# Kernel tuning notes

Hardware: AMD Instinct MI355X
Metric: run time of the kernel (lower is better)

Reference implementation:

```python
import jax, jax.numpy as jnp
import numpy as np

D_MODEL = 1024
NUM_HEADS = 16
D_HEAD = D_MODEL // NUM_HEADS
THETA = 10000.0
NEG_INF = -1e9


def apply_rope(x, theta=THETA):
    # x: (..., S, Dh) with interleaved pairs (2i, 2i+1)
    S, Dh = x.shape[-2], x.shape[-1]
    inv_freq = 1.0 / (theta ** (jnp.arange(0, Dh, 2, dtype=jnp.float32) / Dh))  # (Dh/2,)
    ang = jnp.arange(S, dtype=jnp.float32)[:, None] * inv_freq[None, :]          # (S, Dh/2)
    cos, sin = jnp.cos(ang), jnp.sin(ang)
    x1 = x[..., 0::2]
    x2 = x[..., 1::2]
    r1 = x1 * cos - x2 * sin
    r2 = x1 * sin + x2 * cos
    # interleave back
    return jnp.stack([r1, r2], axis=-1).reshape(x.shape)


def setup_inputs() -> dict:
    key = jax.random.key(0)
    ks = jax.random.split(key, 5)
    B, S = 2, 2048
    scale = 1.0 / np.sqrt(D_MODEL)
    return {
        "x": jax.random.normal(ks[0], (B, S, D_MODEL), dtype=jnp.float32),
        "Wq": jax.random.normal(ks[1], (D_MODEL, D_MODEL), dtype=jnp.float32) * scale,
        "Wk": jax.random.normal(ks[2], (D_MODEL, D_MODEL), dtype=jnp.float32) * scale,
        "Wv": jax.random.normal(ks[3], (D_MODEL, D_MODEL), dtype=jnp.float32) * scale,
        "Wo": jax.random.normal(ks[4], (D_MODEL, D_MODEL), dtype=jnp.float32) * scale,
    }


def reference(x, Wq, Wk, Wv, Wo):
    B, S, _ = x.shape
    def split_heads(t):
        return t.reshape(B, S, NUM_HEADS, D_HEAD).transpose(0, 2, 1, 3)  # (B,H,S,Dh)
    # nn.Linear(bias=False): y = x @ W.T
    Q = split_heads(x @ Wq.T)
    K = split_heads(x @ Wk.T)
    V = split_heads(x @ Wv.T)
    Q = apply_rope(Q)
    K = apply_rope(K)
    scale = 1.0 / jnp.sqrt(jnp.asarray(D_HEAD, dtype=x.dtype))
    scores = jnp.einsum("bhqd,bhkd->bhqk", Q, K) * scale  # (B,H,S,S)
    causal = jnp.tril(jnp.ones((S, S), dtype=bool))
    scores = jnp.where(causal, scores, NEG_INF)
    attn = jax.nn.softmax(scores, axis=-1)
    out = jnp.einsum("bhqk,bhkd->bhqd", attn, V)
    out = out.transpose(0, 2, 1, 3).reshape(B, S, D_MODEL)
    return out @ Wo.T
```

## Files before the change

### kernel.cpp

```cpp
#include <hip/hip_runtime.h>
#include <hip/hip_bf16.h>
#include <stdint.h>

typedef __attribute__((ext_vector_type(8))) short bf8;
typedef __attribute__((ext_vector_type(4))) float f4;

#define MFMA16(a, b, c) __builtin_amdgcn_mfma_f32_16x16x32_bf16((a), (b), (c), 0, 0, 0)

static __device__ __forceinline__ short f2b(float f) {
  uint32_t x = __float_as_uint(f);
  x += 0x7fffu + ((x >> 16) & 1u);
  return (short)(x >> 16);
}

static __device__ __forceinline__ uint32_t pk2(float a, float b) {
  return ((__float_as_uint(a) + 0x8000u) >> 16) |
         ((__float_as_uint(b) + 0x8000u) & 0xffff0000u);
}

static __device__ __forceinline__ void gload16(const short* g, void* l) {
  __builtin_amdgcn_global_load_lds(
      (const __attribute__((address_space(1))) void*)g,
      (__attribute__((address_space(3))) void*)l, 16, 0, 0);
}

__global__ void convert_kernel(const float* __restrict__ x,
                               const float* __restrict__ wq, const float* __restrict__ wk,
                               const float* __restrict__ wv, const float* __restrict__ wo,
                               short* __restrict__ xb, short* __restrict__ Wb,
                               float2* __restrict__ tab) {
  const int bid = blockIdx.x;
  if (bid >= 4096) {
    const int t = (bid - 4096) * 256 + threadIdx.x;
    const int s = t >> 5, i = t & 31;
    const float inv = powf(10000.0f, -(float)i * (1.0f / 32.0f));
    const float ang = (float)s * inv;
    float sv, cv;
    sincosf(ang, &sv, &cv);
    tab[t] = make_float2(cv, sv);
    return;
  }
  const size_t i = ((size_t)bid * 256 + threadIdx.x) * 8;
  const float* __restrict__ src;
  short* __restrict__ dst;
  if (i < 4194304u) {
    src = x + i;
    dst = xb + i;
  } else {
    const size_t j = i - 4194304u;
    const int z = (int)(j >> 20);
    const size_t o = j & 1048575u;
    src = (z == 0 ? wq : z == 1 ? wk : z == 2 ? wv : wo) + o;
    dst = Wb + j;
  }
  const float4 a = *(const float4*)src;
  const float4 b = *(const float4*)(src + 4);
  bf8 v;
  v[0] = f2b(a.x); v[1] = f2b(a.y); v[2] = f2b(a.z); v[3] = f2b(a.w);
  v[4] = f2b(b.x); v[5] = f2b(b.y); v[6] = f2b(b.z); v[7] = f2b(b.w);
  *(bf8*)dst = v;
}

template <int MODE>
__launch_bounds__(256, 2)
__global__ void gemm_kernel(const short* __restrict__ Ab, const short* __restrict__ Wb,
                            short* __restrict__ Qo, short* __restrict__ Ko,
                            short* __restrict__ VTo, float* __restrict__ Fo,
                            const float2* __restrict__ rope) {
  constexpr int K = 1024;
  const int bm = blockIdx.x, bn = blockIdx.y;
  const int z = (MODE == 0) ? blockIdx.z : 3;
  const short* __restrict__ Bb = Wb + ((size_t)z << 20);

  __shared__ short As[128 * 64];
  __shared__ short Bs[128 * 64];

  const int tid = threadIdx.x;
  const int lane = tid & 63;
  const int wave = tid >> 6;
  const int wr = wave >> 1, wc = wave & 1;
  const int lg = lane >> 4, lr = lane & 15;

  f4 acc[4][4];
#pragma unroll
  for (int i = 0; i < 4; i++)
#pragma unroll
    for (int j = 0; j < 4; j++) {
      acc[i][j][0] = 0.f; acc[i][j][1] = 0.f;
      acc[i][j][2] = 0.f; acc[i][j][3] = 0.f;
    }

  const int kc = tid & 7;
  const int srow = tid >> 3;
  const int kcs = (kc ^ (srow & 7)) * 8;
  char* const Asw = (char*)As + wave * 1024;
  char* const Bsw = (char*)Bs + wave * 1024;

  for (int k0 = 0; k0 < K; k0 += 64) {
#pragma unroll
    for (int i = 0; i < 4; i++) {
      const int row = srow + i * 32;
      gload16(Ab + (size_t)(bm * 128 + row) * K + k0 + kcs, Asw + i * 4096);
      gload16(Bb + (size_t)(bn * 128 + row) * K + k0 + kcs, Bsw + i * 4096);
    }
    __syncthreads();
#pragma unroll
    for (int kk = 0; kk < 2; kk++) {
      bf8 af[4], bb[4];
#pragma unroll
      for (int mi = 0; mi < 4; mi++) {
        const int row = wr * 64 + mi * 16 + lr;
        const int lb = (row * 128 + kk * 64 + lg * 16) ^ ((row & 7) << 4);
        af[mi] = *(const bf8*)((const char*)As + lb);
      }
#pragma unroll
      for (int ni = 0; ni < 4; ni++) {
        const int row = wc * 64 + ni * 16 + lr;
        const int lb = (row * 128 + kk * 64 + lg * 16) ^ ((row & 7) << 4);
        bb[ni] = *(const bf8*)((const char*)Bs + lb);
      }
#pragma unroll
      for (int mi = 0; mi < 4; mi++)
#pragma unroll
        for (int ni = 0; ni < 4; ni++)
          acc[mi][ni] = MFMA16(af[mi], bb[ni], acc[mi][ni]);
    }
    __syncthreads();
  }

  if (MODE == 1) {
#pragma unroll
    for (int mi = 0; mi < 4; mi++) {
      const int m0 = bm * 128 + wr * 64 + mi * 16 + lg * 4;
#pragma unroll
      for (int ni = 0; ni < 4; ni++) {
        const int n = bn * 128 + wc * 64 + ni * 16 + lr;
#pragma unroll
        for (int r = 0; r < 4; r++)
          Fo[(size_t)(m0 + r) * 1024 + n] = acc[mi][ni][r];
      }
    }
    return;
  }

  if (z == 2) {
#pragma unroll
    for (int mi = 0; mi < 4; mi++) {
      const int m0 = bm * 128 + wr * 64 + mi * 16 + lg * 4;
      const int b = m0 >> 11, s0 = m0 & 2047;
#pragma unroll
      for (int ni = 0; ni < 4; ni++) {
        const int n = bn * 128 + wc * 64 + ni * 16 + lr;
        ushort4 pk;
        pk.x = (unsigned short)f2b(acc[mi][ni][0]);
        pk.y = (unsigned short)f2b(acc[mi][ni][1]);
        pk.z = (unsigned short)f2b(acc[mi][ni][2]);
        pk.w = (unsigned short)f2b(acc[mi][ni][3]);
        *(ushort4*)(VTo + ((size_t)((b * 16 + (n >> 6)) * 64 + (n & 63))) * 2048 + s0) = pk;
      }
    }
  } else {
    short* __restrict__ Out = (z == 0) ? Qo : Ko;
    const float qscale = (z == 0) ? 0.18033688011112042f : 1.0f;
#pragma unroll
    for (int mi = 0; mi < 4; mi++) {
      const int m0 = bm * 128 + wr * 64 + mi * 16 + lg * 4;
      const int b = m0 >> 11, s0 = m0 & 2047;
#pragma unroll
      for (int ni = 0; ni < 4; ni++) {
        const int n = bn * 128 + wc * 64 + ni * 16 + lr;
        const int h = n >> 6, d = n & 63;
        const float sgn = (d & 1) ? 1.0f : -1.0f;
#pragma unroll
        for (int r = 0; r < 4; r++) {
          const float v = acc[mi][ni][r];
          const float p = __shfl_xor(v, 1);
          const float2 cs = rope[((s0 + r) << 5) + (d >> 1)];
          const float res = (v * cs.x + sgn * p * cs.y) * qscale;
          Out[((size_t)(b * 16 + h) * 2048 + (s0 + r)) * 64 + d] = f2b(res);
        }
      }
    }
  }
}

__launch_bounds__(512, 4)
__global__ void attn_kernel(const short* __restrict__ Qg, const short* __restrict__ Kg,
                            const short* __restrict__ Vg, short* __restrict__ AO) {
  const int S = 2048;
  const int id = blockIdx.x;
  const int xcd = id & 7, slot = id >> 3;
  const int bh = xcd * 4 + (slot & 3);
  const int u = id >> 5;
  const int qb = (u < 8) ? (15 - 2 * u) : (2 * u - 16);
  const int tid = threadIdx.x;
  const int lane = tid & 63, wave = tid >> 6;
  const int lg = lane >> 4, lr = lane & 15;
  const short* __restrict__ Qp = Qg + (size_t)bh * S * 64;
  const short* __restrict__ Kp = Kg + (size_t)bh * S * 64;
  const short* __restrict__ Vp = Vg + (size_t)bh * 64 * S;

  __shared__ short KB[2][64 * 64];
  __shared__ short VB[2][64 * 64];
  __shared__ short PB[8][16 * 64];

  const int srow = tid >> 3;
  const int kcs = ((tid & 7) ^ (srow & 7)) * 8;
  const size_t ksrc = (size_t)srow * 64 + kcs;
  const size_t vsrc = (size_t)srow * 2048 + kcs;

  const int qbase = qb * 128 + wave * 16;
  const int my_nkv = (qbase + 79) >> 6;
  const int blk_nkv = (qb * 128 + 191) >> 6;

  bf8 qf[2];
#pragma unroll
  for (int ks = 0; ks < 2; ks++)
    qf[ks] = *(const bf8*)(Qp + (size_t)(qbase + lr) * 64 + ks * 32 + lg * 8);

  f4 o[4];
#pragma unroll
  for (int dt = 0; dt < 4; dt++) {
    o[dt][0] = 0.f; o[dt][1] = 0.f; o[dt][2] = 0.f; o[dt][3] = 0.f;
  }
  float mrun = -1e30f, lsum = 0.f;

  char* const Pw = (char*)&PB[wave][0];
  const int rowoff = lr * 128;
  const int sw = (lr & 7) << 4;

  gload16(Kp + ksrc, (char*)KB[0] + wave * 1024);
  gload16(Vp + vsrc, (char*)VB[0] + wave * 1024);
  __syncthreads();

  for (int kb = 0; kb < blk_nkv; kb++) {
    const int kvb = kb * 64;
    const int cur = kb & 1;

    if (kb + 1 < blk_nkv) {
      gload16(Kp + (size_t)(kvb + 64) * 64 + ksrc, (char*)KB[cur ^ 1] + wave * 1024);
      gload16(Vp + (size_t)(kvb + 64) + vsrc, (char*)VB[cur ^ 1] + wave * 1024);
    }

    if (kb < my_nkv) {
      const char* Kc = (const char*)KB[cur];
      const char* Vc = (const char*)VB[cur];

      f4 st[4];
      __builtin_amdgcn_s_setprio(1);
#pragma unroll
      for (int nt = 0; nt < 4; nt++) {
        const int row = nt * 16 + lr;
        const int base = row * 128 + lg * 16;
        const int rsw = (row & 7) << 4;
        const bf8 k0 = *(const bf8*)(Kc + ((base) ^ rsw));
        const bf8 k1 = *(const bf8*)(Kc + ((base + 64) ^ rsw));
        f4 c;
        c[0] = 0.f; c[1] = 0.f; c[2] = 0.f; c[3] = 0.f;
        c = MFMA16(k0, qf[0], c);
        c = MFMA16(k1, qf[1], c);
        st[nt] = c;
      }
      __builtin_amdgcn_s_setprio(0);

      if ((kvb + 63) > qbase) {
        const int q = qbase + lr;
#pragma unroll
        for (int nt = 0; nt < 4; nt++)
#pragma unroll
          for (int r = 0; r < 4; r++) {
            const int kv = kvb + nt * 16 + lg * 4 + r;
            if (kv > q) st[nt][r] = -1e9f;
          }
      }

      float m0 = fmaxf(fmaxf(st[0][0], st[0][1]), fmaxf(st[0][2], st[0][3]));
#pragma unroll
      for (int nt = 1; nt < 4; nt++)
        m0 = fmaxf(m0, fmaxf(fmaxf(st[nt][0], st[nt][1]), fmaxf(st[nt][2], st[nt][3])));
      m0 = fmaxf(m0, __shfl_xor(m0, 16));
      m0 = fmaxf(m0, __shfl_xor(m0, 32));

      if (__any(m0 - mrun > 8.0f)) {
        const float mn = fmaxf(mrun, m0);
        const float corr = __builtin_amdgcn_exp2f(mrun - mn);
        mrun = mn;
        lsum *= corr;
#pragma unroll
        for (int r = 0; r < 4; r++) {
          const float co = __shfl(corr, (lg << 2) + r);
#pragma unroll
          for (int dt = 0; dt < 4; dt++) o[dt][r] *= co;
        }
      }

      asm volatile("s_waitcnt lgkmcnt(0)" ::: "memory");

#pragma unroll
      for (int nt = 0; nt < 4; nt++) {
        const float p0 = __builtin_amdgcn_exp2f(st[nt][0] - mrun);
        const float p1 = __builtin_amdgcn_exp2f(st[nt][1] - mrun);
        const float p2 = __builtin_amdgcn_exp2f(st[nt][2] - mrun);
        const float p3 = __builtin_amdgcn_exp2f(st[nt][3] - mrun);
        lsum += (p0 + p1) + (p2 + p3);
        *(uint2*)(Pw + ((rowoff + nt * 32 + lg * 8) ^ sw)) = make_uint2(pk2(p0, p1), pk2(p2, p3));
      }

      asm volatile("s_waitcnt lgkmcnt(0)" ::: "memory");

      bf8 pf[2];
#pragma unroll
      for (int ks = 0; ks < 2; ks++)
        pf[ks] = *(const bf8*)(Pw + ((rowoff + ks * 64 + lg * 16) ^ sw));

      __builtin_amdgcn_s_setprio(1);
#pragma unroll
      for (int dt = 0; dt < 4; dt++) {
        const int row = dt * 16 + lr;
        const int base = row * 128 + lg * 16;
        const int rsw = (row & 7) << 4;
        const bf8 v0 = *(const bf8*)(Vc + ((base) ^ rsw));
        const bf8 v1 = *(const bf8*)(Vc + ((base + 64) ^ rsw));
        o[dt] = MFMA16(pf[0], v0, o[dt]);
        o[dt] = MFMA16(pf[1], v1, o[dt]);
      }
      __builtin_amdgcn_s_setprio(0);
    }

    __syncthreads();
  }

  float s = lsum;
  s += __shfl_xor(s, 16);
  s += __shfl_xor(s, 32);
  const float inv = 1.0f / s;
  float inv_o[4];
#pragma unroll
  for (int r = 0; r < 4; r++) inv_o[r] = __shfl(inv, (lg << 2) + r);

  const int b = bh >> 4, h = bh & 15;
#pragma unroll
  for (int r = 0; r < 4; r++) {
    const int q = qbase + lg * 4 + r;
#pragma unroll
    for (int dt = 0; dt < 4; dt++) {
      const int d = dt * 16 + lr;
      AO[((size_t)b * 2048 + q) * 1024 + h * 64 + d] = f2b(o[dt][r] * inv_o[r]);
    }
  }
}

extern "C" void kernel_launch(void* const* d_in, const int* in_sizes, int n_in,
                              void* d_out, int out_size, void* d_ws, size_t ws_size,
                              hipStream_t stream) {
  const float* x  = (const float*)d_in[0];
  const float* wq = (const float*)d_in[1];
  const float* wk = (const float*)d_in[2];
  const float* wv = (const float*)d_in[3];
  const float* wo = (const float*)d_in[4];
  float* out = (float*)d_out;

  char* ws = (char*)d_ws;
  short*  Qb  = (short*)(ws);
  short*  Kb  = (short*)(ws + (8ull  << 20));
  short*  VTb = (short*)(ws + (16ull << 20));
  short*  AOb = (short*)(ws + (24ull << 20));
  short*  xb  = AOb;
  short*  Wb  = (short*)(ws + (32ull << 20));
  float2* tab = (float2*)(ws + (40ull << 20));

  convert_kernel<<<4352, 256, 0, stream>>>(x, wq, wk, wv, wo, xb, Wb, tab);
  gemm_kernel<0><<<dim3(32, 8, 3), 256, 0, stream>>>(
      xb, Wb, Qb, Kb, VTb, nullptr, tab);
  attn_kernel<<<512, 512, 0, stream>>>(Qb, Kb, VTb, AOb);
  gemm_kernel<1><<<dim3(32, 8, 1), 256, 0, stream>>>(
      AOb, Wb, nullptr, nullptr, nullptr, out, nullptr);
}
```

Baseline: 114.1 us.

## Rewrite attention with 32x32 MFMA, register-resident P via permlane swap

The attention kernel switches from 16x16x32 MFMAs with a shared-memory round trip for the probability tile to 32x32x16 MFMAs. The P tile stays in registers and is rearranged into operand layout with v_permlane32_swap. Blocks shrink to two waves covering 64 query rows each, with a 1024-block grid ordered heaviest-first. The aim is to cut LDS traffic and waits and raise MFMA efficiency. The cost is more accumulator registers and smaller blocks, each doing more K/V staging per wave.

```diff
diff --git a/kernel.cpp b/kernel.cpp
--- a/kernel.cpp
+++ b/kernel.cpp
@@ -4,8 +4,11 @@
 
 typedef __attribute__((ext_vector_type(8))) short bf8;
 typedef __attribute__((ext_vector_type(4))) float f4;
+typedef __attribute__((ext_vector_type(16))) float f16f;
+typedef __attribute__((ext_vector_type(4))) unsigned int u32x4;
 
 #define MFMA16(a, b, c) __builtin_amdgcn_mfma_f32_16x16x32_bf16((a), (b), (c), 0, 0, 0)
+#define MFMA32(a, b, c) __builtin_amdgcn_mfma_f32_32x32x16_bf16((a), (b), (c), 0, 0, 0)
 
 static __device__ __forceinline__ short f2b(float f) {
   uint32_t x = __float_as_uint(f);
@@ -16,6 +19,13 @@
 static __device__ __forceinline__ uint32_t pk2(float a, float b) {
   return ((__float_as_uint(a) + 0x8000u) >> 16) |
          ((__float_as_uint(b) + 0x8000u) & 0xffff0000u);
+}
+
+static __device__ __forceinline__ bf8 mk_bf8(uint32_t w0, uint32_t w1,
+                                             uint32_t w2, uint32_t w3) {
+  union { u32x4 u; bf8 b; } t;
+  t.u = (u32x4){w0, w1, w2, w3};
+  return t.b;
 }
 
 static __device__ __forceinline__ void gload16(const short* g, void* l) {
@@ -184,170 +194,157 @@
   }
 }
 
-__launch_bounds__(512, 4)
+__launch_bounds__(128, 2)
 __global__ void attn_kernel(const short* __restrict__ Qg, const short* __restrict__ Kg,
                             const short* __restrict__ Vg, short* __restrict__ AO) {
   const int S = 2048;
   const int id = blockIdx.x;
-  const int xcd = id & 7, slot = id >> 3;
-  const int bh = xcd * 4 + (slot & 3);
-  const int u = id >> 5;
-  const int qb = (u < 8) ? (15 - 2 * u) : (2 * u - 16);
+  const int xcd = id & 7;
+  const int rest = id >> 3;
+  const int bh = xcd * 4 + (rest & 3);
+  const int qt = 31 - (rest >> 2);
   const int tid = threadIdx.x;
   const int lane = tid & 63, wave = tid >> 6;
-  const int lg = lane >> 4, lr = lane & 15;
+  const int l31 = lane & 31, hi = lane >> 5;
   const short* __restrict__ Qp = Qg + (size_t)bh * S * 64;
   const short* __restrict__ Kp = Kg + (size_t)bh * S * 64;
   const short* __restrict__ Vp = Vg + (size_t)bh * 64 * S;
 
   __shared__ short KB[2][64 * 64];
   __shared__ short VB[2][64 * 64];
-  __shared__ short PB[8][16 * 64];
-
-  const int srow = tid >> 3;
-  const int kcs = ((tid & 7) ^ (srow & 7)) * 8;
-  const size_t ksrc = (size_t)srow * 64 + kcs;
-  const size_t vsrc = (size_t)srow * 2048 + kcs;
-
-  const int qbase = qb * 128 + wave * 16;
-  const int my_nkv = (qbase + 79) >> 6;
-  const int blk_nkv = (qb * 128 + 191) >> 6;
-
-  bf8 qf[2];
-#pragma unroll
-  for (int ks = 0; ks < 2; ks++)
-    qf[ks] = *(const bf8*)(Qp + (size_t)(qbase + lr) * 64 + ks * 32 + lg * 8);
-
-  f4 o[4];
-#pragma unroll
-  for (int dt = 0; dt < 4; dt++) {
-    o[dt][0] = 0.f; o[dt][1] = 0.f; o[dt][2] = 0.f; o[dt][3] = 0.f;
-  }
+
+  const int qbase = qt * 64 + wave * 32;
+  const int nkv = qt + 1;
+
+  const int srow = lane >> 3;
+  const int chsw = ((lane & 7) ^ srow) * 8;
+
+#define STAGE(buf, kvb_)                                                          \
+  do {                                                                            \
+    _Pragma("unroll") for (int c = 0; c < 4; c++) {                               \
+      const int rr = wave * 32 + c * 8 + srow;                                    \
+      gload16(Kp + (size_t)((kvb_) + rr) * 64 + chsw,                             \
+              (char*)KB[buf] + (wave * 32 + c * 8) * 128);                        \
+      gload16(Vp + (size_t)rr * 2048 + (kvb_) + chsw,                             \
+              (char*)VB[buf] + (wave * 32 + c * 8) * 128);                        \
+    }                                                                             \
+  } while (0)
+
+  bf8 qf[4];
+#pragma unroll
+  for (int ks = 0; ks < 4; ks++)
+    qf[ks] = *(const bf8*)(Qp + (size_t)(qbase + l31) * 64 + ks * 16 + hi * 8);
+
+  f16f o0, o1;
+#pragma unroll
+  for (int i = 0; i < 16; i++) { o0[i] = 0.f; o1[i] = 0.f; }
   float mrun = -1e30f, lsum = 0.f;
 
-  char* const Pw = (char*)&PB[wave][0];
-  const int rowoff = lr * 128;
-  const int sw = (lr & 7) << 4;
-
-  gload16(Kp + ksrc, (char*)KB[0] + wave * 1024);
-  gload16(Vp + vsrc, (char*)VB[0] + wave * 1024);
+  const int rsw = (l31 & 7) << 4;
+
+  STAGE(0, 0);
   __syncthreads();
 
-  for (int kb = 0; kb < blk_nkv; kb++) {
+  for (int kb = 0; kb < nkv; kb++) {
     const int kvb = kb * 64;
     const int cur = kb & 1;
 
-    if (kb + 1 < blk_nkv) {
-      gload16(Kp + (size_t)(kvb + 64) * 64 + ksrc, (char*)KB[cur ^ 1] + wave * 1024);
-      gload16(Vp + (size_t)(kvb + 64) + vsrc, (char*)VB[cur ^ 1] + wave * 1024);
-    }
-
-    if (kb < my_nkv) {
-      const char* Kc = (const char*)KB[cur];
-      const char* Vc = (const char*)VB[cur];
-
-      f4 st[4];
-      __builtin_amdgcn_s_setprio(1);
-#pragma unroll
-      for (int nt = 0; nt < 4; nt++) {
-        const int row = nt * 16 + lr;
-        const int base = row * 128 + lg * 16;
-        const int rsw = (row & 7) << 4;
-        const bf8 k0 = *(const bf8*)(Kc + ((base) ^ rsw));
-        const bf8 k1 = *(const bf8*)(Kc + ((base + 64) ^ rsw));
-        f4 c;
-        c[0] = 0.f; c[1] = 0.f; c[2] = 0.f; c[3] = 0.f;
-        c = MFMA16(k0, qf[0], c);
-        c = MFMA16(k1, qf[1], c);
-        st[nt] = c;
-      }
-      __builtin_amdgcn_s_setprio(0);
-
-      if ((kvb + 63) > qbase) {
-        const int q = qbase + lr;
-#pragma unroll
-        for (int nt = 0; nt < 4; nt++)
-#pragma unroll
-          for (int r = 0; r < 4; r++) {
-            const int kv = kvb + nt * 16 + lg * 4 + r;
-            if (kv > q) st[nt][r] = -1e9f;
-          }
-      }
-
-      float m0 = fmaxf(fmaxf(st[0][0], st[0][1]), fmaxf(st[0][2], st[0][3]));
-#pragma unroll
-      for (int nt = 1; nt < 4; nt++)
-        m0 = fmaxf(m0, fmaxf(fmaxf(st[nt][0], st[nt][1]), fmaxf(st[nt][2], st[nt][3])));
-      m0 = fmaxf(m0, __shfl_xor(m0, 16));
-      m0 = fmaxf(m0, __shfl_xor(m0, 32));
-
-      if (__any(m0 - mrun > 8.0f)) {
-        const float mn = fmaxf(mrun, m0);
-        const float corr = __builtin_amdgcn_exp2f(mrun - mn);
-        mrun = mn;
-        lsum *= corr;
-#pragma unroll
-        for (int r = 0; r < 4; r++) {
-          const float co = __shfl(corr, (lg << 2) + r);
-#pragma unroll
-          for (int dt = 0; dt < 4; dt++) o[dt][r] *= co;
-        }
-      }
-
-      asm volatile("s_waitcnt lgkmcnt(0)" ::: "memory");
-
-#pragma unroll
-      for (int nt = 0; nt < 4; nt++) {
-        const float p0 = __builtin_amdgcn_exp2f(st[nt][0] - mrun);
-        const float p1 = __builtin_amdgcn_exp2f(st[nt][1] - mrun);
-        const float p2 = __builtin_amdgcn_exp2f(st[nt][2] - mrun);
-        const float p3 = __builtin_amdgcn_exp2f(st[nt][3] - mrun);
-        lsum += (p0 + p1) + (p2 + p3);
-        *(uint2*)(Pw + ((rowoff + nt * 32 + lg * 8) ^ sw)) = make_uint2(pk2(p0, p1), pk2(p2, p3));
-      }
-
-      asm volatile("s_waitcnt lgkmcnt(0)" ::: "memory");
-
-      bf8 pf[2];
-#pragma unroll
-      for (int ks = 0; ks < 2; ks++)
-        pf[ks] = *(const bf8*)(Pw + ((rowoff + ks * 64 + lg * 16) ^ sw));
-
-      __builtin_amdgcn_s_setprio(1);
-#pragma unroll
-      for (int dt = 0; dt < 4; dt++) {
-        const int row = dt * 16 + lr;
-        const int base = row * 128 + lg * 16;
-        const int rsw = (row & 7) << 4;
-        const bf8 v0 = *(const bf8*)(Vc + ((base) ^ rsw));
-        const bf8 v1 = *(const bf8*)(Vc + ((base + 64) ^ rsw));
-        o[dt] = MFMA16(pf[0], v0, o[dt]);
-        o[dt] = MFMA16(pf[1], v1, o[dt]);
-      }
-      __builtin_amdgcn_s_setprio(0);
-    }
+    if (kb + 1 < nkv) STAGE(cur ^ 1, kvb + 64);
+
+    const char* Kc = (const char*)KB[cur];
+    const char* Vc = (const char*)VB[cur];
+
+    f16f st0, st1;
+#pragma unroll
+    for (int i = 0; i < 16; i++) { st0[i] = 0.f; st1[i] = 0.f; }
+    __builtin_amdgcn_s_setprio(1);
+#pragma unroll
+    for (int ks = 0; ks < 4; ks++) {
+      const int off = ks * 32 + hi * 16;
+      const bf8 k0 = *(const bf8*)(Kc + l31 * 128 + (off ^ rsw));
+      const bf8 k1 = *(const bf8*)(Kc + (32 + l31) * 128 + (off ^ rsw));
+      st0 = MFMA32(k0, qf[ks], st0);
+      st1 = MFMA32(k1, qf[ks], st1);
+    }
+    __builtin_amdgcn_s_setprio(0);
+
+    if (kvb + 63 > qbase) {
+      const int q = qbase + l31;
+#pragma unroll
+      for (int reg = 0; reg < 16; reg++) {
+        const int kv = kvb + (reg & 3) + 8 * (reg >> 2) + 4 * hi;
+        if (kv > q) st0[reg] = -1e9f;
+        if (kv + 32 > q) st1[reg] = -1e9f;
+      }
+    }
+
+    float m0 = fmaxf(st0[0], st1[0]);
+#pragma unroll
+    for (int reg = 1; reg < 16; reg++) m0 = fmaxf(m0, fmaxf(st0[reg], st1[reg]));
+    m0 = fmaxf(m0, __shfl_xor(m0, 32));
+
+    if (__any(m0 - mrun > 8.0f)) {
+      const float mn = fmaxf(mrun, m0);
+      const float corr = __builtin_amdgcn_exp2f(mrun - mn);
+      mrun = mn;
+      lsum *= corr;
+#pragma unroll
+      for (int reg = 0; reg < 16; reg++) {
+        const int qo = (reg & 3) + 8 * (reg >> 2) + 4 * hi;
+        const float co = __shfl(corr, qo);
+        o0[reg] *= co;
+        o1[reg] *= co;
+      }
+    }
+
+#pragma unroll
+    for (int reg = 0; reg < 16; reg++) {
+      st0[reg] = __builtin_amdgcn_exp2f(st0[reg] - mrun);
+      st1[reg] = __builtin_amdgcn_exp2f(st1[reg] - mrun);
+      lsum += st0[reg] + st1[reg];
+    }
+
+    bf8 pa[4];
+#pragma unroll
+    for (int k2 = 0; k2 < 4; k2++) {
+      const f16f& pn = (k2 < 2) ? st0 : st1;
+      const int bs = (k2 & 1) * 8;
+      uint32_t x0 = pk2(pn[bs + 0], pn[bs + 1]);
+      uint32_t y0 = pk2(pn[bs + 4], pn[bs + 5]);
+      uint32_t x1 = pk2(pn[bs + 2], pn[bs + 3]);
+      uint32_t y1 = pk2(pn[bs + 6], pn[bs + 7]);
+      asm volatile("v_permlane32_swap_b32 %0, %1" : "+v"(x0), "+v"(y0));
+      asm volatile("v_permlane32_swap_b32 %0, %1" : "+v"(x1), "+v"(y1));
+      pa[k2] = mk_bf8(x0, x1, y0, y1);
+    }
+
+    __builtin_amdgcn_s_setprio(1);
+#pragma unroll
+    for (int k2 = 0; k2 < 4; k2++) {
+      const int off = k2 * 32 + hi * 16;
+      const bf8 v0 = *(const bf8*)(Vc + l31 * 128 + (off ^ rsw));
+      const bf8 v1 = *(const bf8*)(Vc + (32 + l31) * 128 + (off ^ rsw));
+      o0 = MFMA32(pa[k2], v0, o0);
+      o1 = MFMA32(pa[k2], v1, o1);
+    }
+    __builtin_amdgcn_s_setprio(0);
 
     __syncthreads();
   }
 
-  float s = lsum;
-  s += __shfl_xor(s, 16);
-  s += __shfl_xor(s, 32);
+  const float s = lsum + __shfl_xor(lsum, 32);
   const float inv = 1.0f / s;
-  float inv_o[4];
-#pragma unroll
-  for (int r = 0; r < 4; r++) inv_o[r] = __shfl(inv, (lg << 2) + r);
-
   const int b = bh >> 4, h = bh & 15;
 #pragma unroll
-  for (int r = 0; r < 4; r++) {
-    const int q = qbase + lg * 4 + r;
-#pragma unroll
-    for (int dt = 0; dt < 4; dt++) {
-      const int d = dt * 16 + lr;
-      AO[((size_t)b * 2048 + q) * 1024 + h * 64 + d] = f2b(o[dt][r] * inv_o[r]);
-    }
-  }
+  for (int reg = 0; reg < 16; reg++) {
+    const int qo = (reg & 3) + 8 * (reg >> 2) + 4 * hi;
+    const float io = __shfl(inv, qo);
+    const int q = qbase + qo;
+    const size_t base = ((size_t)b * 2048 + q) * 1024 + h * 64 + l31;
+    AO[base] = f2b(o0[reg] * io);
+    AO[base + 32] = f2b(o1[reg] * io);
+  }
+#undef STAGE
 }
 
 extern "C" void kernel_launch(void* const* d_in, const int* in_sizes, int n_in,
@@ -372,7 +369,7 @@
   convert_kernel<<<4352, 256, 0, stream>>>(x, wq, wk, wv, wo, xb, Wb, tab);
   gemm_kernel<0><<<dim3(32, 8, 3), 256, 0, stream>>>(
       xb, Wb, Qb, Kb, VTb, nullptr, tab);
-  attn_kernel<<<512, 512, 0, stream>>>(Qb, Kb, VTb, AOb);
+  attn_kernel<<<1024, 128, 0, stream>>>(Qb, Kb, VTb, AOb);
   gemm_kernel<1><<<dim3(32, 8, 1), 256, 0, stream>>>(
       AOb, Wb, nullptr, nullptr, nullptr, out, nullptr);
 }
```

New measurement: 118.6 us. 1.04x slower.

## Make attention kernel persistent with atomic work queue and 64-row query tiles

Applied to the files above, without the earlier changes.

Changes the attention kernel from a fixed grid of 512-thread blocks, each handling a 128-row query tile, to persistent 256-thread blocks. Each block pulls work items from a global atomic counter, taking the heaviest causal tiles first (largest query block index first), so load balance is set at run time rather than by a static block-to-tile mapping. With smaller tiles, waves no longer sit idle on key/value blocks that lie past their causal limit. The counter is reset inside the conversion kernel. In exchange it adds an atomic and a block barrier per work item, issues more load instructions per thread for each K/V tile, and reuses loaded K/V across fewer query rows.

```diff
diff --git a/kernel.cpp b/kernel.cpp
--- a/kernel.cpp
+++ b/kernel.cpp
@@ -28,10 +28,11 @@
                                const float* __restrict__ wq, const float* __restrict__ wk,
                                const float* __restrict__ wv, const float* __restrict__ wo,
                                short* __restrict__ xb, short* __restrict__ Wb,
-                               float2* __restrict__ tab) {
+                               float2* __restrict__ tab, unsigned int* __restrict__ ctr) {
   const int bid = blockIdx.x;
   if (bid >= 4096) {
     const int t = (bid - 4096) * 256 + threadIdx.x;
+    if (t == 0) *ctr = 0u;
     const int s = t >> 5, i = t & 31;
     const float inv = powf(10000.0f, -(float)i * (1.0f / 32.0f));
     const float ang = (float)s * inv;
@@ -184,65 +185,70 @@
   }
 }
 
-__launch_bounds__(512, 4)
+__launch_bounds__(256, 2)
 __global__ void attn_kernel(const short* __restrict__ Qg, const short* __restrict__ Kg,
-                            const short* __restrict__ Vg, short* __restrict__ AO) {
+                            const short* __restrict__ Vg, short* __restrict__ AO,
+                            unsigned int* __restrict__ ctr) {
   const int S = 2048;
-  const int id = blockIdx.x;
-  const int xcd = id & 7, slot = id >> 3;
-  const int bh = xcd * 4 + (slot & 3);
-  const int u = id >> 5;
-  const int qb = (u < 8) ? (15 - 2 * u) : (2 * u - 16);
   const int tid = threadIdx.x;
   const int lane = tid & 63, wave = tid >> 6;
   const int lg = lane >> 4, lr = lane & 15;
-  const short* __restrict__ Qp = Qg + (size_t)bh * S * 64;
-  const short* __restrict__ Kp = Kg + (size_t)bh * S * 64;
-  const short* __restrict__ Vp = Vg + (size_t)bh * 64 * S;
 
   __shared__ short KB[2][64 * 64];
   __shared__ short VB[2][64 * 64];
-  __shared__ short PB[8][16 * 64];
+  __shared__ short PB[4][16 * 64];
+  __shared__ int s_u;
 
   const int srow = tid >> 3;
   const int kcs = ((tid & 7) ^ (srow & 7)) * 8;
-  const size_t ksrc = (size_t)srow * 64 + kcs;
-  const size_t vsrc = (size_t)srow * 2048 + kcs;
-
-  const int qbase = qb * 128 + wave * 16;
-  const int my_nkv = (qbase + 79) >> 6;
-  const int blk_nkv = (qb * 128 + 191) >> 6;
-
-  bf8 qf[2];
-#pragma unroll
-  for (int ks = 0; ks < 2; ks++)
-    qf[ks] = *(const bf8*)(Qp + (size_t)(qbase + lr) * 64 + ks * 32 + lg * 8);
-
-  f4 o[4];
-#pragma unroll
-  for (int dt = 0; dt < 4; dt++) {
-    o[dt][0] = 0.f; o[dt][1] = 0.f; o[dt][2] = 0.f; o[dt][3] = 0.f;
-  }
-  float mrun = -1e30f, lsum = 0.f;
-
-  char* const Pw = (char*)&PB[wave][0];
   const int rowoff = lr * 128;
   const int sw = (lr & 7) << 4;
-
-  gload16(Kp + ksrc, (char*)KB[0] + wave * 1024);
-  gload16(Vp + vsrc, (char*)VB[0] + wave * 1024);
-  __syncthreads();
-
-  for (int kb = 0; kb < blk_nkv; kb++) {
-    const int kvb = kb * 64;
-    const int cur = kb & 1;
-
-    if (kb + 1 < blk_nkv) {
-      gload16(Kp + (size_t)(kvb + 64) * 64 + ksrc, (char*)KB[cur ^ 1] + wave * 1024);
-      gload16(Vp + (size_t)(kvb + 64) + vsrc, (char*)VB[cur ^ 1] + wave * 1024);
-    }
-
-    if (kb < my_nkv) {
+  char* const Pw = (char*)&PB[wave][0];
+
+  for (;;) {
+    if (tid == 0) s_u = (int)atomicAdd(ctr, 1u);
+    __syncthreads();
+    const int u = s_u;
+    if (u >= 1024) break;
+    const int qb = 31 - (u >> 5);
+    const int bh = u & 31;
+    const short* __restrict__ Qp = Qg + (size_t)bh * S * 64;
+    const short* __restrict__ Kp = Kg + (size_t)bh * S * 64;
+    const short* __restrict__ Vp = Vg + (size_t)bh * 64 * S;
+
+    const int qbase = qb * 64 + wave * 16;
+    const int nkv = qb + 1;
+
+    bf8 qf[2];
+#pragma unroll
+    for (int ks = 0; ks < 2; ks++)
+      qf[ks] = *(const bf8*)(Qp + (size_t)(qbase + lr) * 64 + ks * 32 + lg * 8);
+
+    f4 o[4];
+#pragma unroll
+    for (int dt = 0; dt < 4; dt++) {
+      o[dt][0] = 0.f; o[dt][1] = 0.f; o[dt][2] = 0.f; o[dt][3] = 0.f;
+    }
+    float mrun = -1e30f, lsum = 0.f;
+
+    gload16(Kp + (size_t)srow * 64 + kcs, (char*)KB[0] + wave * 1024);
+    gload16(Kp + (size_t)(32 + srow) * 64 + kcs, (char*)KB[0] + 4096 + wave * 1024);
+    gload16(Vp + (size_t)srow * 2048 + kcs, (char*)VB[0] + wave * 1024);
+    gload16(Vp + (size_t)(32 + srow) * 2048 + kcs, (char*)VB[0] + 4096 + wave * 1024);
+    __syncthreads();
+
+    for (int kb = 0; kb < nkv; kb++) {
+      const int kvb = kb * 64;
+      const int cur = kb & 1;
+
+      if (kb + 1 < nkv) {
+        const int nb = kvb + 64;
+        gload16(Kp + (size_t)(nb + srow) * 64 + kcs, (char*)KB[cur ^ 1] + wave * 1024);
+        gload16(Kp + (size_t)(nb + 32 + srow) * 64 + kcs, (char*)KB[cur ^ 1] + 4096 + wave * 1024);
+        gload16(Vp + (size_t)srow * 2048 + nb + kcs, (char*)VB[cur ^ 1] + wave * 1024);
+        gload16(Vp + (size_t)(32 + srow) * 2048 + nb + kcs, (char*)VB[cur ^ 1] + 4096 + wave * 1024);
+      }
+
       const char* Kc = (const char*)KB[cur];
       const char* Vc = (const char*)VB[cur];
 
@@ -253,7 +259,7 @@
         const int row = nt * 16 + lr;
         const int base = row * 128 + lg * 16;
         const int rsw = (row & 7) << 4;
-        const bf8 k0 = *(const bf8*)(Kc + ((base) ^ rsw));
+        const bf8 k0 = *(const bf8*)(Kc + (base ^ rsw));
         const bf8 k1 = *(const bf8*)(Kc + ((base + 64) ^ rsw));
         f4 c;
         c[0] = 0.f; c[1] = 0.f; c[2] = 0.f; c[3] = 0.f;
@@ -319,33 +325,33 @@
         const int row = dt * 16 + lr;
         const int base = row * 128 + lg * 16;
         const int rsw = (row & 7) << 4;
-        const bf8 v0 = *(const bf8*)(Vc + ((base) ^ rsw));
+        const bf8 v0 = *(const bf8*)(Vc + (base ^ rsw));
         const bf8 v1 = *(const bf8*)(Vc + ((base + 64) ^ rsw));
         o[dt] = MFMA16(pf[0], v0, o[dt]);
         o[dt] = MFMA16(pf[1], v1, o[dt]);
       }
       __builtin_amdgcn_s_setprio(0);
-    }
-
-    __syncthreads();
-  }
-
-  float s = lsum;
-  s += __shfl_xor(s, 16);
-  s += __shfl_xor(s, 32);
-  const float inv = 1.0f / s;
-  float inv_o[4];
-#pragma unroll
-  for (int r = 0; r < 4; r++) inv_o[r] = __shfl(inv, (lg << 2) + r);
-
-  const int b = bh >> 4, h = bh & 15;
-#pragma unroll
-  for (int r = 0; r < 4; r++) {
-    const int q = qbase + lg * 4 + r;
-#pragma unroll
-    for (int dt = 0; dt < 4; dt++) {
-      const int d = dt * 16 + lr;
-      AO[((size_t)b * 2048 + q) * 1024 + h * 64 + d] = f2b(o[dt][r] * inv_o[r]);
+
+      __syncthreads();
+    }
+
+    float s = lsum;
+    s += __shfl_xor(s, 16);
+    s += __shfl_xor(s, 32);
+    const float inv = 1.0f / s;
+    float inv_o[4];
+#pragma unroll
+    for (int r = 0; r < 4; r++) inv_o[r] = __shfl(inv, (lg << 2) + r);
+
+    const int b = bh >> 4, h = bh & 15;
+#pragma unroll
+    for (int r = 0; r < 4; r++) {
+      const int q = qbase + lg * 4 + r;
+#pragma unroll
+      for (int dt = 0; dt < 4; dt++) {
+        const int d = dt * 16 + lr;
+        AO[((size_t)b * 2048 + q) * 1024 + h * 64 + d] = f2b(o[dt][r] * inv_o[r]);
+      }
     }
   }
 }
@@ -368,11 +374,12 @@
   short*  xb  = AOb;
   short*  Wb  = (short*)(ws + (32ull << 20));
   float2* tab = (float2*)(ws + (40ull << 20));
-
-  convert_kernel<<<4352, 256, 0, stream>>>(x, wq, wk, wv, wo, xb, Wb, tab);
+  unsigned int* ctr = (unsigned int*)(ws + (40ull << 20) + (512u << 10));
+
+  convert_kernel<<<4352, 256, 0, stream>>>(x, wq, wk, wv, wo, xb, Wb, tab, ctr);
   gemm_kernel<0><<<dim3(32, 8, 3), 256, 0, stream>>>(
       xb, Wb, Qb, Kb, VTb, nullptr, tab);
-  attn_kernel<<<512, 512, 0, stream>>>(Qb, Kb, VTb, AOb);
+  attn_kernel<<<512, 256, 0, stream>>>(Qb, Kb, VTb, AOb, ctr);
   gemm_kernel<1><<<dim3(32, 8, 1), 256, 0, stream>>>(
       AOb, Wb, nullptr, nullptr, nullptr, out, nullptr);
 }
```

Result: slower. 120.6 us (+5.7%).

## Stage 128-row KV tiles per barrier and simplify q-block scheduling order

Applied to the files above, without the earlier changes.

The attention kernel now loads two 64-row K/V sub-tiles (128 rows) per double-buffered stage, so each __syncthreads covers twice as much work. This halves the number of barriers and outer iterations but doubles the K/V shared memory footprint, which may lower occupancy. The q-block assignment also changes from an interleaved heavy/light ordering to a simple descending order across slots, which alters load balance across workgroups.

```diff
diff --git a/kernel.cpp b/kernel.cpp
--- a/kernel.cpp
+++ b/kernel.cpp
@@ -191,8 +191,7 @@
   const int id = blockIdx.x;
   const int xcd = id & 7, slot = id >> 3;
   const int bh = xcd * 4 + (slot & 3);
-  const int u = id >> 5;
-  const int qb = (u < 8) ? (15 - 2 * u) : (2 * u - 16);
+  const int qb = 15 - (slot >> 2);
   const int tid = threadIdx.x;
   const int lane = tid & 63, wave = tid >> 6;
   const int lg = lane >> 4, lr = lane & 15;
@@ -200,18 +199,15 @@
   const short* __restrict__ Kp = Kg + (size_t)bh * S * 64;
   const short* __restrict__ Vp = Vg + (size_t)bh * 64 * S;
 
-  __shared__ short KB[2][64 * 64];
-  __shared__ short VB[2][64 * 64];
+  __shared__ short KB[2][2][64 * 64];
+  __shared__ short VB[2][2][64 * 64];
   __shared__ short PB[8][16 * 64];
 
   const int srow = tid >> 3;
   const int kcs = ((tid & 7) ^ (srow & 7)) * 8;
-  const size_t ksrc = (size_t)srow * 64 + kcs;
-  const size_t vsrc = (size_t)srow * 2048 + kcs;
 
   const int qbase = qb * 128 + wave * 16;
-  const int my_nkv = (qbase + 79) >> 6;
-  const int blk_nkv = (qb * 128 + 191) >> 6;
+  const int nkv = qb + 1;
 
   bf8 qf[2];
 #pragma unroll
@@ -229,102 +225,113 @@
   const int rowoff = lr * 128;
   const int sw = (lr & 7) << 4;
 
-  gload16(Kp + ksrc, (char*)KB[0] + wave * 1024);
-  gload16(Vp + vsrc, (char*)VB[0] + wave * 1024);
+#pragma unroll
+  for (int h = 0; h < 2; h++) {
+    gload16(Kp + (size_t)(64 * h + srow) * 64 + kcs, (char*)KB[0][h] + wave * 1024);
+    gload16(Vp + (size_t)srow * 2048 + 64 * h + kcs, (char*)VB[0][h] + wave * 1024);
+  }
   __syncthreads();
 
-  for (int kb = 0; kb < blk_nkv; kb++) {
-    const int kvb = kb * 64;
+  for (int kb = 0; kb < nkv; kb++) {
+    const int kvb = kb * 128;
     const int cur = kb & 1;
 
-    if (kb + 1 < blk_nkv) {
-      gload16(Kp + (size_t)(kvb + 64) * 64 + ksrc, (char*)KB[cur ^ 1] + wave * 1024);
-      gload16(Vp + (size_t)(kvb + 64) + vsrc, (char*)VB[cur ^ 1] + wave * 1024);
-    }
-
-    if (kb < my_nkv) {
-      const char* Kc = (const char*)KB[cur];
-      const char* Vc = (const char*)VB[cur];
-
-      f4 st[4];
-      __builtin_amdgcn_s_setprio(1);
-#pragma unroll
-      for (int nt = 0; nt < 4; nt++) {
-        const int row = nt * 16 + lr;
-        const int base = row * 128 + lg * 16;
-        const int rsw = (row & 7) << 4;
-        const bf8 k0 = *(const bf8*)(Kc + ((base) ^ rsw));
-        const bf8 k1 = *(const bf8*)(Kc + ((base + 64) ^ rsw));
-        f4 c;
-        c[0] = 0.f; c[1] = 0.f; c[2] = 0.f; c[3] = 0.f;
-        c = MFMA16(k0, qf[0], c);
-        c = MFMA16(k1, qf[1], c);
-        st[nt] = c;
-      }
-      __builtin_amdgcn_s_setprio(0);
-
-      if ((kvb + 63) > qbase) {
-        const int q = qbase + lr;
-#pragma unroll
-        for (int nt = 0; nt < 4; nt++)
+    if (kb + 1 < nkv) {
+      const int nb = kvb + 128;
+#pragma unroll
+      for (int h = 0; h < 2; h++) {
+        gload16(Kp + (size_t)(nb + 64 * h + srow) * 64 + kcs, (char*)KB[cur ^ 1][h] + wave * 1024);
+        gload16(Vp + (size_t)srow * 2048 + nb + 64 * h + kcs, (char*)VB[cur ^ 1][h] + wave * 1024);
+      }
+    }
+
+#pragma unroll
+    for (int h = 0; h < 2; h++) {
+      const int kvbh = kvb + 64 * h;
+      if (kvbh < qbase + 16) {
+        const char* Kc = (const char*)KB[cur][h];
+        const char* Vc = (const char*)VB[cur][h];
+
+        f4 st[4];
+        __builtin_amdgcn_s_setprio(1);
+#pragma unroll
+        for (int nt = 0; nt < 4; nt++) {
+          const int row = nt * 16 + lr;
+          const int base = row * 128 + lg * 16;
+          const int rsw = (row & 7) << 4;
+          const bf8 k0 = *(const bf8*)(Kc + (base ^ rsw));
+          const bf8 k1 = *(const bf8*)(Kc + ((base + 64) ^ rsw));
+          f4 c;
+          c[0] = 0.f; c[1] = 0.f; c[2] = 0.f; c[3] = 0.f;
+          c = MFMA16(k0, qf[0], c);
+          c = MFMA16(k1, qf[1], c);
+          st[nt] = c;
+        }
+        __builtin_amdgcn_s_setprio(0);
+
+        if ((kvbh + 63) > qbase) {
+          const int q = qbase + lr;
+#pragma unroll
+          for (int nt = 0; nt < 4; nt++)
+#pragma unroll
+            for (int r = 0; r < 4; r++) {
+              const int kv = kvbh + nt * 16 + lg * 4 + r;
+              if (kv > q) st[nt][r] = -1e9f;
+            }
+        }
+
+        float m0 = fmaxf(fmaxf(st[0][0], st[0][1]), fmaxf(st[0][2], st[0][3]));
+#pragma unroll
+        for (int nt = 1; nt < 4; nt++)
+          m0 = fmaxf(m0, fmaxf(fmaxf(st[nt][0], st[nt][1]), fmaxf(st[nt][2], st[nt][3])));
+        m0 = fmaxf(m0, __shfl_xor(m0, 16));
+        m0 = fmaxf(m0, __shfl_xor(m0, 32));
+
+        if (__any(m0 - mrun > 8.0f)) {
+          const float mn = fmaxf(mrun, m0);
+          const float corr = __builtin_amdgcn_exp2f(mrun - mn);
+          mrun = mn;
+          lsum *= corr;
 #pragma unroll
           for (int r = 0; r < 4; r++) {
-            const int kv = kvb + nt * 16 + lg * 4 + r;
-            if (kv > q) st[nt][r] = -1e9f;
+            const float co = __shfl(corr, (lg << 2) + r);
+#pragma unroll
+            for (int dt = 0; dt < 4; dt++) o[dt][r] *= co;
           }
-      }
-
-      float m0 = fmaxf(fmaxf(st[0][0], st[0][1]), fmaxf(st[0][2], st[0][3]));
-#pragma unroll
-      for (int nt = 1; nt < 4; nt++)
-        m0 = fmaxf(m0, fmaxf(fmaxf(st[nt][0], st[nt][1]), fmaxf(st[nt][2], st[nt][3])));
-      m0 = fmaxf(m0, __shfl_xor(m0, 16));
-      m0 = fmaxf(m0, __shfl_xor(m0, 32));
-
-      if (__any(m0 - mrun > 8.0f)) {
-        const float mn = fmaxf(mrun, m0);
-        const float corr = __builtin_amdgcn_exp2f(mrun - mn);
-        mrun = mn;
-        lsum *= corr;
-#pragma unroll
-        for (int r = 0; r < 4; r++) {
-          const float co = __shfl(corr, (lg << 2) + r);
-#pragma unroll
-          for (int dt = 0; dt < 4; dt++) o[dt][r] *= co;
-        }
-      }
-
-      asm volatile("s_waitcnt lgkmcnt(0)" ::: "memory");
-
-#pragma unroll
-      for (int nt = 0; nt < 4; nt++) {
-        const float p0 = __builtin_amdgcn_exp2f(st[nt][0] - mrun);
-        const float p1 = __builtin_amdgcn_exp2f(st[nt][1] - mrun);
-        const float p2 = __builtin_amdgcn_exp2f(st[nt][2] - mrun);
-        const float p3 = __builtin_amdgcn_exp2f(st[nt][3] - mrun);
-        lsum += (p0 + p1) + (p2 + p3);
-        *(uint2*)(Pw + ((rowoff + nt * 32 + lg * 8) ^ sw)) = make_uint2(pk2(p0, p1), pk2(p2, p3));
-      }
-
-      asm volatile("s_waitcnt lgkmcnt(0)" ::: "memory");
-
-      bf8 pf[2];
-#pragma unroll
-      for (int ks = 0; ks < 2; ks++)
-        pf[ks] = *(const bf8*)(Pw + ((rowoff + ks * 64 + lg * 16) ^ sw));
-
-      __builtin_amdgcn_s_setprio(1);
-#pragma unroll
-      for (int dt = 0; dt < 4; dt++) {
-        const int row = dt * 16 + lr;
-        const int base = row * 128 + lg * 16;
-        const int rsw = (row & 7) << 4;
-        const bf8 v0 = *(const bf8*)(Vc + ((base) ^ rsw));
-        const bf8 v1 = *(const bf8*)(Vc + ((base + 64) ^ rsw));
-        o[dt] = MFMA16(pf[0], v0, o[dt]);
-        o[dt] = MFMA16(pf[1], v1, o[dt]);
-      }
-      __builtin_amdgcn_s_setprio(0);
+        }
+
+        asm volatile("s_waitcnt lgkmcnt(0)" ::: "memory");
+
+#pragma unroll
+        for (int nt = 0; nt < 4; nt++) {
+          const float p0 = __builtin_amdgcn_exp2f(st[nt][0] - mrun);
+          const float p1 = __builtin_amdgcn_exp2f(st[nt][1] - mrun);
+          const float p2 = __builtin_amdgcn_exp2f(st[nt][2] - mrun);
+          const float p3 = __builtin_amdgcn_exp2f(st[nt][3] - mrun);
+          lsum += (p0 + p1) + (p2 + p3);
+          *(uint2*)(Pw + ((rowoff + nt * 32 + lg * 8) ^ sw)) = make_uint2(pk2(p0, p1), pk2(p2, p3));
+        }
+
+        asm volatile("s_waitcnt lgkmcnt(0)" ::: "memory");
+
+        bf8 pf[2];
+#pragma unroll
+        for (int ks = 0; ks < 2; ks++)
+          pf[ks] = *(const bf8*)(Pw + ((rowoff + ks * 64 + lg * 16) ^ sw));
+
+        __builtin_amdgcn_s_setprio(1);
+#pragma unroll
+        for (int dt = 0; dt < 4; dt++) {
+          const int row = dt * 16 + lr;
+          const int base = row * 128 + lg * 16;
+          const int rsw = (row & 7) << 4;
+          const bf8 v0 = *(const bf8*)(Vc + (base ^ rsw));
+          const bf8 v1 = *(const bf8*)(Vc + ((base + 64) ^ rsw));
+          o[dt] = MFMA16(pf[0], v0, o[dt]);
+          o[dt] = MFMA16(pf[1], v1, o[dt]);
+        }
+        __builtin_amdgcn_s_setprio(0);
+      }
     }
 
     __syncthreads();
```

Measured after the change: 110.8 us. 1.03x faster.
